# Kernel optimization log

Measured on AMD Instinct MI355X. Metric: run time of the kernel, lower is better.

## Reference

```python
import jax, jax.numpy as jnp
import numpy as np

KS = 5
STRIDE = 1


def extract_patches(x, ks, s):
    # TF tf.image.extract_patches ordering: (row, col, channel) flattened
    B, H, W, C = x.shape
    oh = (H - ks) // s + 1
    ow = (W - ks) // s + 1
    cols = [x[:, i:i + (oh - 1) * s + 1:s, j:j + (ow - 1) * s + 1:s, :]
            for i in range(ks) for j in range(ks)]
    p = jnp.stack(cols, axis=3)  # [B, oh, ow, ks*ks, C]
    return p.reshape(B, oh * ow, ks * ks * C)


def setup_inputs() -> dict:
    key = jax.random.key(0)
    k1, k2, k3 = jax.random.split(key, 3)
    B, H, W, C, K = 32, 14, 14, 32, 64
    mu_in = jax.random.normal(k1, (B, H, W, C), dtype=jnp.float32)
    Sigma_in = jax.random.uniform(k2, (B, H * W, H * W, C), dtype=jnp.float32)
    w_mu = 0.05 * jax.random.normal(k3, (KS, KS, C, K), dtype=jnp.float32)
    w_sigma = jnp.full((K,), -2.2, dtype=jnp.float32)
    return {"mu_in": mu_in, "Sigma_in": Sigma_in, "w_mu": w_mu, "w_sigma": w_sigma}


def reference(mu_in, Sigma_in, w_mu, w_sigma):
    B, H, W, C = mu_in.shape
    ks = w_mu.shape[0]
    K = w_mu.shape[-1]
    s = STRIDE

    # mean path: standard conv2d, NHWC / HWIO
    mu_out = jax.lax.conv_general_dilated(
        mu_in, w_mu, (s, s), 'VALID',
        dimension_numbers=('NHWC', 'HWIO', 'NHWC'))

    # diag of Sigma_in over the two N dims: [B,N,N,C] -> [B,C,N] -> [B,H,W,C]
    diag_sigma = jnp.diagonal(Sigma_in, axis1=1, axis2=2)           # [B,C,N]
    diag_sigma = jnp.transpose(diag_sigma, (0, 2, 1)).reshape(B, H, W, C)

    dsg = extract_patches(diag_sigma, ks, s)                        # [B,P,M]
    P = dsg.shape[1]

    mu_cov_sq = (w_mu * w_mu).reshape(-1, K)                        # [M,K]
    v1 = dsg @ mu_cov_sq                                            # [B,P,K]

    sp = jnp.log1p(jnp.exp(w_sigma))                                # softplus, [K]
    tr = jnp.sum(dsg, axis=2, keepdims=True)                        # [B,P,1]
    diag_vals = v1 + sp[None, None, :] * tr                         # [B,P,K] (trace1 + mu_wT_sigmags_mu_w diags)

    mu_p = extract_patches(mu_in, ks, s)                            # [B,P,M]
    G = jnp.einsum('bpm,bqm->bpq', mu_p, mu_p)                      # [B,P,P]

    Sigma_out = sp[None, None, None, :] * G[..., None]              # [B,P,P,K]
    ip = jnp.arange(P)
    Sigma_out = Sigma_out.at[:, ip, ip, :].add(diag_vals)

    Sigma_out = jnp.where(jnp.isnan(Sigma_out), 0.0, Sigma_out)
    Sigma_out = jnp.where(jnp.isinf(Sigma_out), 0.0, Sigma_out)

    # TF set_diag acts on the LAST two dims ([P,K] inner matrices) -- reproduce exactly
    m = min(P, K)
    ii = jnp.arange(m)
    Sigma_out = Sigma_out.at[:, :, ii, ii].set(jnp.abs(Sigma_out[:, :, ii, ii]))
    return mu_out, Sigma_out
```

## Files before the change

### kernel.cpp

```cpp
#include <hip/hip_runtime.h>
#include <cmath>

typedef __attribute__((ext_vector_type(8))) short short8;
typedef __attribute__((ext_vector_type(4))) float f32x4;

#define NB 32
#define MU_OUT_SZ (NB*100*64)
#define LDAP 56

__device__ inline unsigned short f2bf(float f) {
  unsigned u = __builtin_bit_cast(unsigned, f);
  u += 0x7fffu + ((u >> 16) & 1u);
  return (unsigned short)(u >> 16);
}

__global__ __launch_bounds__(256) void prepW(
    const float* __restrict__ w_mu, const float* __restrict__ w_sigma,
    unsigned short* __restrict__ wf) {
  __shared__ float wsh[2048];
  const int ij = blockIdx.x, t = threadIdx.x;
  const float4* src = (const float4*)(w_mu + (size_t)ij * 2048);
  ((float4*)wsh)[t]       = src[t];
  ((float4*)wsh)[t + 256] = src[t + 256];
  __syncthreads();
#pragma unroll
  for (int id0 = 0; id0 < 512; id0 += 256) {
    const int id = id0 + t;
    const int kind = id >> 8;
    const int rest = id & 255;
    const int n = rest >> 6, l = rest & 63;
    const int col = n * 16 + (l & 15);
    const int m0 = (l >> 4) * 8;
    const float sp = log1pf(expf(w_sigma[col]));
    unsigned short v[8];
#pragma unroll
    for (int i = 0; i < 8; ++i) {
      const float wv = wsh[(m0 + i) * 64 + col];
      const float x = kind ? (wv * wv + sp) : wv;
      v[i] = f2bf(x);
    }
    uint4 pk;
    pk.x = v[0] | ((unsigned)v[1] << 16);
    pk.y = v[2] | ((unsigned)v[3] << 16);
    pk.z = v[4] | ((unsigned)v[5] << 16);
    pk.w = v[6] | ((unsigned)v[7] << 16);
    *(uint4*)(wf + (size_t)((ij * 8 + kind * 4 + n) * 64 + l) * 8) = pk;
  }
}

__global__ __launch_bounds__(512) void fusedH(
    const float* __restrict__ mu_in, const float* __restrict__ Sigma_in,
    const unsigned short* __restrict__ wf, const float* __restrict__ w_sigma,
    float* __restrict__ out) {
  __shared__ unsigned short mu_sh[196 * LDAP];
  __shared__ unsigned short sd_sh[196 * LDAP];
  __shared__ float g_sh[16][64];
  __shared__ float dv_sh[16][64];
  const int r = blockIdx.x;
  const int zh = blockIdx.y;
  const int b = blockIdx.z;
  const int t = threadIdx.x, l = t & 63, w = t >> 6;
  const int p0 = r * 16;
  const bool hasDv = (zh == 0) ? (r <= 3) : (r >= 4);

  const float4* mu4 = (const float4*)(mu_in + (size_t)b * 6272);
  for (int f = t; f < 1568; f += 512) {
    const float4 v = mu4[f];
    const int row = f >> 3, c = (f & 7) * 4;
    ushort4 pv;
    pv.x = f2bf(v.x); pv.y = f2bf(v.y); pv.z = f2bf(v.z); pv.w = f2bf(v.w);
    *(ushort4*)(mu_sh + row * LDAP + c) = pv;
  }
  if (hasDv) {
    for (int f = t; f < 1568; f += 512) {
      const int row = f >> 3, c = (f & 7) * 4;
      const float4 s = *(const float4*)(Sigma_in +
          ((size_t)(b * 196 + row) * 196 + row) * 32 + c);
      ushort4 ps;
      ps.x = f2bf(s.x); ps.y = f2bf(s.y); ps.z = f2bf(s.z); ps.w = f2bf(s.w);
      *(ushort4*)(sd_sh + row * LDAP + c) = ps;
    }
  }
  __syncthreads();

  const int laneP = l & 15, g16 = (l >> 4) * 8;
  const int pA = (p0 + laneP > 99) ? 99 : p0 + laneP;
  const int baseA = ((pA / 10) * 14 + (pA % 10)) * LDAP + g16;
  const int gT = (zh == 0) ? ((w < 4) ? w : -1) : ((w < 3) ? 4 + w : -1);
  const int sn = (zh == 0) ? ((w >= 4) ? w - 4 : -1)
                           : ((w >= 3 && w < 7) ? w - 3 : -1);
  int qg = 0, baseB = 0;
  if (gT >= 0) {
    qg = gT * 16 + laneP;
    const int qc = qg > 99 ? 99 : qg;
    baseB = ((qc / 10) * 14 + (qc % 10)) * LDAP + g16;
  }
  const int kslot = (sn >= 0) ? (hasDv ? 4 + sn : sn) : 0;

  const short8* wfp = (const short8*)wf;
  short8 fw = {};
  if (sn >= 0) fw = wfp[(size_t)kslot * 64 + l];
  f32x4 aG = {}, aX = {};
  for (int ij = 0; ij < 25; ++ij) {
    short8 fw_n = fw;
    if (sn >= 0 && ij < 24) fw_n = wfp[(size_t)((ij + 1) * 8 + kslot) * 64 + l];
    const int off = ((ij / 5) * 14 + (ij % 5)) * LDAP;
    if (gT >= 0) {
      const short8 fA = *(const short8*)(mu_sh + baseA + off);
      const short8 fB = *(const short8*)(mu_sh + baseB + off);
      aG = __builtin_amdgcn_mfma_f32_16x16x32_bf16(fA, fB, aG, 0, 0, 0);
    }
    if (sn >= 0) {
      if (hasDv) {
        const short8 fS = *(const short8*)(sd_sh + baseA + off);
        aX = __builtin_amdgcn_mfma_f32_16x16x32_bf16(fS, fw, aX, 0, 0, 0);
      } else {
        const short8 fA = *(const short8*)(mu_sh + baseA + off);
        aX = __builtin_amdgcn_mfma_f32_16x16x32_bf16(fA, fw, aX, 0, 0, 0);
      }
    }
    fw = fw_n;
  }

  const int prow0 = (l >> 4) * 4;
  if (gT >= 0 && qg < 100) {
    const int ql = qg - zh * 64;
#pragma unroll
    for (int j = 0; j < 4; ++j) g_sh[prow0 + j][ql] = aG[j];
  }
  if (sn >= 0) {
    const int k = sn * 16 + laneP;
    if (hasDv) {
#pragma unroll
      for (int j = 0; j < 4; ++j) dv_sh[prow0 + j][k] = aX[j];
    } else {
      float* mo = out + (size_t)b * 6400;
#pragma unroll
      for (int j = 0; j < 4; ++j) {
        const int p = p0 + prow0 + j;
        if (p < 100) mo[p * 64 + k] = aX[j];
      }
    }
  }
  __syncthreads();

  const int nrows = (r == 6) ? 4 : 16;
  const int k4 = (t & 15) * 4;
  const float4 wsv = *(const float4*)(w_sigma + k4);
  f32x4 sp4;
  sp4.x = log1pf(expf(wsv.x));
  sp4.y = log1pf(expf(wsv.y));
  sp4.z = log1pf(expf(wsv.z));
  sp4.w = log1pf(expf(wsv.w));
  float* sig0 = out + MU_OUT_SZ + (size_t)(b * 100 + p0) * 6400 + zh * 64 * 64;

  if (zh == 0) {
    for (int row = 0; row < nrows; ++row) {
      const bool dvRow = hasDv && (p0 + row < 64);
      float* rowp = sig0 + (size_t)row * 6400;
#pragma unroll
      for (int s = 0; s < 2; ++s) {
        const int idx = t + s * 512;
        const int ql = idx >> 4;
        const float g = g_sh[row][ql];
        f32x4 v;
        v.x = sp4.x * g; v.y = sp4.y * g; v.z = sp4.z * g; v.w = sp4.w * g;
        if (dvRow && ql == p0 + row) {
          const float4 dvv = *(const float4*)&dv_sh[row][k4];
          v.x += dvv.x; v.y += dvv.y; v.z += dvv.z; v.w += dvv.w;
        }
        v.x = (ql == k4)     ? fabsf(v.x) : v.x;
        v.y = (ql == k4 + 1) ? fabsf(v.y) : v.y;
        v.z = (ql == k4 + 2) ? fabsf(v.z) : v.z;
        v.w = (ql == k4 + 3) ? fabsf(v.w) : v.w;
        __builtin_nontemporal_store(v, (f32x4*)(rowp + (size_t)idx * 4));
      }
    }
  } else {
    for (int row = 0; row < nrows; ++row) {
      float* rowp = sig0 + (size_t)row * 6400;
      for (int idx = t; idx < 576; idx += 512) {
        const int ql = idx >> 4;
        const float g = g_sh[row][ql];
        f32x4 v;
        v.x = sp4.x * g; v.y = sp4.y * g; v.z = sp4.z * g; v.w = sp4.w * g;
        if (hasDv && 64 + ql == p0 + row) {
          const float4 dvv = *(const float4*)&dv_sh[row][k4];
          v.x += dvv.x; v.y += dvv.y; v.z += dvv.z; v.w += dvv.w;
        }
        __builtin_nontemporal_store(v, (f32x4*)(rowp + (size_t)idx * 4));
      }
    }
  }
}

extern "C" void kernel_launch(void* const* d_in, const int* in_sizes, int n_in,
                              void* d_out, int out_size, void* d_ws, size_t ws_size,
                              hipStream_t stream) {
  const float* mu_in    = (const float*)d_in[0];
  const float* Sigma_in = (const float*)d_in[1];
  const float* w_mu     = (const float*)d_in[2];
  const float* w_sigma  = (const float*)d_in[3];
  float* out = (float*)d_out;
  unsigned short* wf = (unsigned short*)d_ws;

  prepW<<<25, 256, 0, stream>>>(w_mu, w_sigma, wf);
  fusedH<<<dim3(7, 2, NB), 512, 0, stream>>>(mu_in, Sigma_in, wf, w_sigma, out);
}
```

Measured before the change: 33.83 us.

## Hoist bf16 conversion of mu and Sigma diagonal into prep kernel via workspace

Moves the fp32-to-bf16 conversion of mu_in and the strided Sigma diagonal gather out of the main kernel and into the prep kernel. Each batch is converted once into the workspace instead of once per (r, zh) block, which was redundant 14x. The main kernel then copies packed bf16 rows into LDS with 16-byte loads. Output stores switch from nontemporal to regular stores. The cost is an extra global round trip through the workspace and a larger prep launch.

Result: faster. 32.57 us (-3.7%).

```diff
diff --git a/kernel.cpp b/kernel.cpp
--- a/kernel.cpp
+++ b/kernel.cpp
@@ -7,6 +7,10 @@
 #define NB 32
 #define MU_OUT_SZ (NB*100*64)
 #define LDAP 56
+
+#define WS_WF 0
+#define WS_MU 204800
+#define WS_SD 606208
 
 __device__ inline unsigned short f2bf(float f) {
   unsigned u = __builtin_bit_cast(unsigned, f);
@@ -14,46 +18,67 @@
   return (unsigned short)(u >> 16);
 }
 
-__global__ __launch_bounds__(256) void prepW(
+__global__ __launch_bounds__(256) void prep(
+    const float* __restrict__ mu_in, const float* __restrict__ Sigma_in,
     const float* __restrict__ w_mu, const float* __restrict__ w_sigma,
-    unsigned short* __restrict__ wf) {
-  __shared__ float wsh[2048];
-  const int ij = blockIdx.x, t = threadIdx.x;
-  const float4* src = (const float4*)(w_mu + (size_t)ij * 2048);
-  ((float4*)wsh)[t]       = src[t];
-  ((float4*)wsh)[t + 256] = src[t + 256];
-  __syncthreads();
-#pragma unroll
-  for (int id0 = 0; id0 < 512; id0 += 256) {
-    const int id = id0 + t;
-    const int kind = id >> 8;
-    const int rest = id & 255;
-    const int n = rest >> 6, l = rest & 63;
-    const int col = n * 16 + (l & 15);
-    const int m0 = (l >> 4) * 8;
-    const float sp = log1pf(expf(w_sigma[col]));
-    unsigned short v[8];
-#pragma unroll
-    for (int i = 0; i < 8; ++i) {
-      const float wv = wsh[(m0 + i) * 64 + col];
-      const float x = kind ? (wv * wv + sp) : wv;
-      v[i] = f2bf(x);
-    }
-    uint4 pk;
-    pk.x = v[0] | ((unsigned)v[1] << 16);
-    pk.y = v[2] | ((unsigned)v[3] << 16);
-    pk.z = v[4] | ((unsigned)v[5] << 16);
-    pk.w = v[6] | ((unsigned)v[7] << 16);
-    *(uint4*)(wf + (size_t)((ij * 8 + kind * 4 + n) * 64 + l) * 8) = pk;
-  }
-}
-
-__global__ __launch_bounds__(512) void fusedH(
-    const float* __restrict__ mu_in, const float* __restrict__ Sigma_in,
-    const unsigned short* __restrict__ wf, const float* __restrict__ w_sigma,
+    unsigned char* __restrict__ ws) {
+  const int blk = blockIdx.x, t = threadIdx.x;
+  if (blk < 25) {
+    __shared__ float wsh[2048];
+    const int ij = blk;
+    unsigned short* wf = (unsigned short*)(ws + WS_WF);
+    const float4* src = (const float4*)(w_mu + (size_t)ij * 2048);
+    ((float4*)wsh)[t]       = src[t];
+    ((float4*)wsh)[t + 256] = src[t + 256];
+    __syncthreads();
+#pragma unroll
+    for (int id0 = 0; id0 < 512; id0 += 256) {
+      const int id = id0 + t;
+      const int kind = id >> 8;
+      const int rest = id & 255;
+      const int n = rest >> 6, l = rest & 63;
+      const int col = n * 16 + (l & 15);
+      const int m0 = (l >> 4) * 8;
+      const float sp = log1pf(expf(w_sigma[col]));
+      unsigned short v[8];
+#pragma unroll
+      for (int i = 0; i < 8; ++i) {
+        const float wv = wsh[(m0 + i) * 64 + col];
+        const float x = kind ? (wv * wv + sp) : wv;
+        v[i] = f2bf(x);
+      }
+      uint4 pk;
+      pk.x = v[0] | ((unsigned)v[1] << 16);
+      pk.y = v[2] | ((unsigned)v[3] << 16);
+      pk.z = v[4] | ((unsigned)v[5] << 16);
+      pk.w = v[6] | ((unsigned)v[7] << 16);
+      *(uint4*)(wf + (size_t)((ij * 8 + kind * 4 + n) * 64 + l) * 8) = pk;
+    }
+  } else {
+    const int b = blk - 25;
+    unsigned short* mub = (unsigned short*)(ws + WS_MU) + (size_t)b * 6272;
+    unsigned short* sdb = (unsigned short*)(ws + WS_SD) + (size_t)b * 6272;
+    const float4* mu4 = (const float4*)(mu_in + (size_t)b * 6272);
+    for (int f = t; f < 1568; f += 256) {
+      const float4 v = mu4[f];
+      ushort4 pv;
+      pv.x = f2bf(v.x); pv.y = f2bf(v.y); pv.z = f2bf(v.z); pv.w = f2bf(v.w);
+      *(ushort4*)(mub + f * 4) = pv;
+      const int n = f >> 3, c = (f & 7) * 4;
+      const float4 s = *(const float4*)(Sigma_in +
+          ((size_t)(b * 196 + n) * 196 + n) * 32 + c);
+      ushort4 ps;
+      ps.x = f2bf(s.x); ps.y = f2bf(s.y); ps.z = f2bf(s.z); ps.w = f2bf(s.w);
+      *(ushort4*)(sdb + f * 4) = ps;
+    }
+  }
+}
+
+__global__ __launch_bounds__(512) void fusedH2(
+    const unsigned char* __restrict__ ws, const float* __restrict__ w_sigma,
     float* __restrict__ out) {
-  __shared__ unsigned short mu_sh[196 * LDAP];
-  __shared__ unsigned short sd_sh[196 * LDAP];
+  __shared__ __align__(16) unsigned short mu_sh[196 * LDAP];
+  __shared__ __align__(16) unsigned short sd_sh[196 * LDAP];
   __shared__ float g_sh[16][64];
   __shared__ float dv_sh[16][64];
   const int r = blockIdx.x;
@@ -63,22 +88,16 @@
   const int p0 = r * 16;
   const bool hasDv = (zh == 0) ? (r <= 3) : (r >= 4);
 
-  const float4* mu4 = (const float4*)(mu_in + (size_t)b * 6272);
-  for (int f = t; f < 1568; f += 512) {
-    const float4 v = mu4[f];
-    const int row = f >> 3, c = (f & 7) * 4;
-    ushort4 pv;
-    pv.x = f2bf(v.x); pv.y = f2bf(v.y); pv.z = f2bf(v.z); pv.w = f2bf(v.w);
-    *(ushort4*)(mu_sh + row * LDAP + c) = pv;
+  const uint4* mus = (const uint4*)((const unsigned short*)(ws + WS_MU) + (size_t)b * 6272);
+  for (int j = t; j < 784; j += 512) {
+    const int n = j >> 2, c = (j & 3) * 8;
+    *(uint4*)(mu_sh + n * LDAP + c) = mus[j];
   }
   if (hasDv) {
-    for (int f = t; f < 1568; f += 512) {
-      const int row = f >> 3, c = (f & 7) * 4;
-      const float4 s = *(const float4*)(Sigma_in +
-          ((size_t)(b * 196 + row) * 196 + row) * 32 + c);
-      ushort4 ps;
-      ps.x = f2bf(s.x); ps.y = f2bf(s.y); ps.z = f2bf(s.z); ps.w = f2bf(s.w);
-      *(ushort4*)(sd_sh + row * LDAP + c) = ps;
+    const uint4* sds = (const uint4*)((const unsigned short*)(ws + WS_SD) + (size_t)b * 6272);
+    for (int j = t; j < 784; j += 512) {
+      const int n = j >> 2, c = (j & 3) * 8;
+      *(uint4*)(sd_sh + n * LDAP + c) = sds[j];
     }
   }
   __syncthreads();
@@ -97,7 +116,7 @@
   }
   const int kslot = (sn >= 0) ? (hasDv ? 4 + sn : sn) : 0;
 
-  const short8* wfp = (const short8*)wf;
+  const short8* wfp = (const short8*)(ws + WS_WF);
   short8 fw = {};
   if (sn >= 0) fw = wfp[(size_t)kslot * 64 + l];
   f32x4 aG = {}, aX = {};
@@ -173,7 +192,7 @@
         v.y = (ql == k4 + 1) ? fabsf(v.y) : v.y;
         v.z = (ql == k4 + 2) ? fabsf(v.z) : v.z;
         v.w = (ql == k4 + 3) ? fabsf(v.w) : v.w;
-        __builtin_nontemporal_store(v, (f32x4*)(rowp + (size_t)idx * 4));
+        *(f32x4*)(rowp + (size_t)idx * 4) = v;
       }
     }
   } else {
@@ -188,7 +207,7 @@
           const float4 dvv = *(const float4*)&dv_sh[row][k4];
           v.x += dvv.x; v.y += dvv.y; v.z += dvv.z; v.w += dvv.w;
         }
-        __builtin_nontemporal_store(v, (f32x4*)(rowp + (size_t)idx * 4));
+        *(f32x4*)(rowp + (size_t)idx * 4) = v;
       }
     }
   }
@@ -202,8 +221,8 @@
   const float* w_mu     = (const float*)d_in[2];
   const float* w_sigma  = (const float*)d_in[3];
   float* out = (float*)d_out;
-  unsigned short* wf = (unsigned short*)d_ws;
-
-  prepW<<<25, 256, 0, stream>>>(w_mu, w_sigma, wf);
-  fusedH<<<dim3(7, 2, NB), 512, 0, stream>>>(mu_in, Sigma_in, wf, w_sigma, out);
-}
+  unsigned char* ws = (unsigned char*)d_ws;
+
+  prep<<<57, 256, 0, stream>>>(mu_in, Sigma_in, w_mu, w_sigma, ws);
+  fusedH2<<<dim3(7, 2, NB), 512, 0, stream>>>(ws, w_sigma, out);
+}
```
